# Kernel tuning notes

Measured on AMD Instinct MI355X. Metric: run time of the kernel, lower is better.

Reference implementation:

```python
import jax, jax.numpy as jnp
import numpy as np

LOG2E = 1.4426950408889634  # 1/ln(2): convert natural-log gates to log2 space (kernel uses exp2)
BT = 64  # chunk size


def setup_inputs() -> dict:
    key = jax.random.key(0)
    ks = jax.random.split(key, 5)
    B, H, T, K, V = 4, 8, 4096, 128, 128
    return {
        "q": jax.random.normal(ks[0], (B, H, T, K), dtype=jnp.float32),
        "k": jax.random.normal(ks[1], (B, H, T, K), dtype=jnp.float32),
        "v": jax.random.normal(ks[2], (B, H, T, V), dtype=jnp.float32),
        "i_gate": jax.random.normal(ks[3], (B, H, T), dtype=jnp.float32),
        "f_gate": jax.random.normal(ks[4], (B, H, T), dtype=jnp.float32),
    }


def reference(q, k, v, i_gate, f_gate):
    B, H, T, K = q.shape
    V = v.shape[-1]
    NT = T // BT
    scale = K ** -0.5

    # gate preprocessing: log-sigmoid forget gate, both gates moved to log2 space
    vecF = jax.nn.log_sigmoid(f_gate) * LOG2E  # [B,H,T]
    vecI = i_gate * LOG2E                      # [B,H,T]

    f_c = vecF.reshape(B, H, NT, BT)
    i_c = vecI.reshape(B, H, NT, BT)
    qc = q.reshape(B, H, NT, BT, K)
    kc = k.reshape(B, H, NT, BT, K)
    vc = v.reshape(B, H, NT, BT, V)

    vecB = jnp.cumsum(f_c, axis=-1)            # inclusive cumsum of f within chunk [B,H,NT,BT]
    scaG = vecB[..., -1]                       # total decay per chunk [B,H,NT]
    vecA = i_c + (scaG[..., None] - vecB)      # i_j + sum of f after j within chunk

    # ---- inter-chunk recurrence over matrix state C, normalizer n, max m ----
    kx = jnp.moveaxis(kc, 2, 0)  # [NT,B,H,BT,K]
    vx = jnp.moveaxis(vc, 2, 0)
    ax = jnp.moveaxis(vecA, 2, 0)  # [NT,B,H,BT]
    gx = jnp.moveaxis(scaG, 2, 0)  # [NT,B,H]

    C0 = jnp.zeros((B, H, K, V), dtype=q.dtype)
    n0 = jnp.zeros((B, H, K), dtype=q.dtype)
    m0 = jnp.zeros((B, H), dtype=q.dtype)

    def step(carry, inp):
        C, n, m = carry
        kk, vv, a, g = inp
        m_next = jnp.maximum(g + m, jnp.max(a, axis=-1))      # running stabilizer max
        dec = jnp.exp2(g + m - m_next)                        # [B,H]
        kbar = kk * jnp.exp2(a - m_next[..., None])[..., None]
        C_next = C * dec[..., None, None] + jnp.einsum('bhtk,bhtv->bhkv', kbar, vv)
        n_next = n * dec[..., None] + kbar.sum(axis=-2)
        return (C_next, n_next, m_next), (C, n, m)

    _, (Cp, np_, mp) = jax.lax.scan(step, (C0, n0, m0), (kx, vx, ax, gx))
    Cp = jnp.moveaxis(Cp, 0, 2)   # state entering each chunk [B,H,NT,K,V]
    np_ = jnp.moveaxis(np_, 0, 2)  # [B,H,NT,K]
    mp = jnp.moveaxis(mp, 0, 2)   # [B,H,NT]

    # ---- intra-chunk parallel part ----
    idx = jnp.arange(BT)
    causal = idx[:, None] >= idx[None, :]  # query i attends key j<=i
    # logD[i,j] = B_i - B_j + I_j for j<=i
    logD = vecB[..., :, None] - vecB[..., None, :] + i_c[..., None, :]
    logD = jnp.where(causal, logD, -jnp.inf)
    m_intra = logD.max(axis=-1)                                   # [B,H,NT,BT]
    m_comb = jnp.maximum(mp[..., None] + vecB, m_intra)           # total stabilizer per row
    D = jnp.exp2(logD - m_comb[..., None])                        # masked entries -> 0

    S = jnp.einsum('bhcik,bhcjk->bhcij', qc, kc) * scale * D
    qbar = qc * (scale * jnp.exp2(vecB + mp[..., None] - m_comb))[..., None]

    Hnum = jnp.einsum('bhcik,bhckv->bhciv', qbar, Cp) + jnp.einsum('bhcij,bhcjv->bhciv', S, vc)
    den = jnp.einsum('bhcik,bhck->bhci', qbar, np_) + S.sum(axis=-1)
    norm = jnp.maximum(jnp.abs(den), jnp.exp2(-m_comb))
    h = Hnum / norm[..., None]
    return h.reshape(B, H, T, V)
```

## Files before the change

kernel.cpp:

```cpp
#include <hip/hip_runtime.h>
#include <hip/hip_bf16.h>
#include <math.h>


#define LOG2E 1.4426950408889634f
constexpr int Bsz = 4, Hsz = 8, Tsz = 4096, Ksz = 128, Vsz = 128;
constexpr int BT = 64, NT = 64, BH = Bsz * Hsz;
constexpr float SCALE = 0.08838834764831845f;
constexpr int GS = 8, NG = NT / GS;

typedef __attribute__((ext_vector_type(8))) short short8v;
typedef __attribute__((ext_vector_type(4))) float f32x4;
typedef __attribute__((ext_vector_type(4))) unsigned short u16x4;
typedef __attribute__((ext_vector_type(8))) unsigned short u16x8;

__device__ inline float bf2f(unsigned short u) {
    union { unsigned int i; float f; } c; c.i = ((unsigned int)u) << 16; return c.f;
}
__device__ inline unsigned short f2bf(float f) {
    __hip_bfloat16 h = __float2bfloat16(f);
    union { __hip_bfloat16 b; unsigned short u; } cv; cv.b = h; return cv.u;
}
__device__ inline float f4c(const float4& v, int y) {
    return y == 0 ? v.x : y == 1 ? v.y : y == 2 ? v.z : v.w;
}

__global__ __launch_bounds__(64) void k_gates(
    const float* __restrict__ ig, const float* __restrict__ fg,
    float* __restrict__ vecB, float* __restrict__ vecI, float* __restrict__ vecA,
    float* __restrict__ mintra, float* __restrict__ scaG, float* __restrict__ scaA)
{
    int c = blockIdx.x, bh = blockIdx.y, lane = threadIdx.x;
    int t = bh * Tsz + c * BT + lane;
    float f = fg[t];
    float ls = fminf(f, 0.f) - log1pf(expf(-fabsf(f)));
    float vF = ls * LOG2E;
    float vI = ig[t] * LOG2E;
    float b = vF;
    #pragma unroll
    for (int off = 1; off < 64; off <<= 1) {
        float o = __shfl_up(b, off, 64);
        if (lane >= off) b += o;
    }
    float g = __shfl(b, 63, 64);
    float mi = vI - b;
    #pragma unroll
    for (int off = 1; off < 64; off <<= 1) {
        float o = __shfl_up(mi, off, 64);
        if (lane >= off) mi = fmaxf(mi, o);
    }
    float a = vI + g - b;
    vecB[t] = b; vecI[t] = vI; vecA[t] = a; mintra[t] = b + mi;
    float am = a;
    #pragma unroll
    for (int off = 32; off; off >>= 1) am = fmaxf(am, __shfl_xor(am, off, 64));
    if (lane == 0) { scaG[bh * NT + c] = g; scaA[bh * NT + c] = am; }
}

__global__ __launch_bounds__(64) void k_mscan(
    const float* __restrict__ scaG, const float* __restrict__ scaA,
    float* __restrict__ mp, float* __restrict__ dec,
    float* __restrict__ pdec, float* __restrict__ decG)
{
    int bh = blockIdx.x, lane = threadIdx.x;
    float g0 = scaG[bh * NT + lane];
    float a = g0, b = scaA[bh * NT + lane];
    #pragma unroll
    for (int off = 1; off < 64; off <<= 1) {
        float ap = __shfl_up(a, off, 64);
        float bp = __shfl_up(b, off, 64);
        if (lane >= off) { b = fmaxf(bp + a, b); a = ap + a; }
    }
    float m_incl = fmaxf(a, b);
    float m_prev = __shfl_up(m_incl, 1, 64);
    if (lane == 0) { m_prev = 0.f; mp[bh * (NT + 1)] = 0.f; }
    mp[bh * (NT + 1) + lane + 1] = m_incl;
    dec[bh * NT + lane] = exp2f(g0 + m_prev - m_incl);
    float cumE = a - g0;
    int gs = lane & ~(GS - 1);
    float cumE_gs = __shfl(cumE, gs, 64);
    float mp_gs   = __shfl(m_prev, gs, 64);
    pdec[bh * NT + lane] = exp2f(cumE - cumE_gs + mp_gs - m_prev);
    int ge = (lane * GS) & 63, gl = (lane * GS + GS - 1) & 63;
    float cumS = __shfl(cumE, ge, 64);
    float mS   = __shfl(m_prev, ge, 64);
    float cumL = __shfl(a, gl, 64);
    float mL   = __shfl(m_incl, gl, 64);
    if (lane < NG) decG[bh * NG + lane] = exp2f(cumL - cumS + mS - mL);
}

__global__ __launch_bounds__(256, 1) void k_state(
    const float* __restrict__ kg, const float* __restrict__ vg,
    const float* __restrict__ vecA, const float* __restrict__ mp,
    const float* __restrict__ dec,
    unsigned short* __restrict__ CpL, unsigned short* __restrict__ Gb,
    float* __restrict__ npl, float* __restrict__ nG)
{
    int g = blockIdx.x, bh = blockIdx.y, tid = threadIdx.x;
    int c0 = g * GS;
    int lane = tid & 63, wid = tid >> 6;
    int lrow = lane & 15, kgrp = lane >> 4;

    __shared__ __align__(16) unsigned short kT[2][128][72];
    __shared__ __align__(16) unsigned short vT[2][128][72];
    __shared__ float nUp[2][128][5];

    int cb = tid & 15, jr = tid >> 4;
    int wboff = (((jr >> 1) ^ (cb & 7)) * 16) + (jr & 1) * 8;
    const float* mpb = mp + bh * (NT + 1);

    float4 kreg[4][2], vreg[4][2];
    auto issue_loads = [&](int cc) {
        size_t hbc = (size_t)bh * Tsz + (size_t)(c0 + cc) * BT;
        #pragma unroll
        for (int x = 0; x < 4; ++x)
            #pragma unroll
            for (int p = 0; p < 2; ++p) {
                kreg[x][p] = *(const float4*)(kg + (hbc + jr * 4 + x) * Ksz + p * 64 + cb * 4);
                vreg[x][p] = *(const float4*)(vg + (hbc + jr * 4 + x) * Vsz + p * 64 + cb * 4);
            }
    };
    auto cvt_store = [&](int cc, int bb) {
        size_t hbc = (size_t)bh * Tsz + (size_t)(c0 + cc) * BT;
        float mpn = mpb[c0 + cc + 1];
        float s4[4];
        #pragma unroll
        for (int x = 0; x < 4; ++x) s4[x] = exp2f(vecA[hbc + jr * 4 + x] - mpn);
        #pragma unroll
        for (int p = 0; p < 2; ++p) {
            int cc0 = p * 64 + cb * 4;
            #pragma unroll
            for (int y = 0; y < 4; ++y) {
                u16x4 h, w;
                float psum = 0.f;
                #pragma unroll
                for (int x = 0; x < 4; ++x) {
                    float kf = f4c(kreg[x][p], y) * s4[x];
                    h[x] = f2bf(kf);
                    psum += kf;
                    w[x] = f2bf(f4c(vreg[x][p], y));
                }
                *(u16x4*)((char*)&kT[bb][cc0 + y][0] + wboff) = h;
                *(u16x4*)((char*)&vT[bb][cc0 + y][0] + wboff) = w;
                psum += __shfl_xor(psum, 16, 64);
                psum += __shfl_xor(psum, 32, 64);
                if (kgrp == 0) nUp[bb][cc0 + y][wid] = psum;
            }
        }
    };

    issue_loads(0);
    cvt_store(0, 0);
    __syncthreads();

    f32x4 acc[2][8];
    #pragma unroll
    for (int kt = 0; kt < 2; ++kt)
        #pragma unroll
        for (int vt = 0; vt < 8; ++vt) acc[kt][vt] = (f32x4){0.f, 0.f, 0.f, 0.f};
    float n_own = 0.f;

    int bb = 0;
    for (int t = 0; t < GS; ++t) {
        if (t + 1 < GS) issue_loads(t + 1);
        int c = c0 + t;
        unsigned short* Cb = CpL + (size_t)(bh * NT + c) * (Ksz * Vsz);
        #pragma unroll
        for (int kt = 0; kt < 2; ++kt) {
            int ktile = wid * 2 + kt;
            #pragma unroll
            for (int vt = 0; vt < 8; ++vt) {
                u16x4 w;
                #pragma unroll
                for (int r = 0; r < 4; ++r) w[r] = f2bf(acc[kt][vt][r]);
                *(u16x4*)(Cb + ((size_t)(ktile * 8 + vt) * 64 + lane) * 4) = w;
            }
        }
        if (tid < Ksz) npl[(size_t)(bh * NT + c) * Ksz + tid] = n_own;
        float dct = dec[bh * NT + c];
        #pragma unroll
        for (int kt = 0; kt < 2; ++kt)
            #pragma unroll
            for (int vt = 0; vt < 8; ++vt)
                #pragma unroll
                for (int r = 0; r < 4; ++r) acc[kt][vt][r] *= dct;
        #pragma unroll
        for (int ks = 0; ks < 2; ++ks) {
            int G2 = ks * 4 + kgrp;
            #pragma unroll
            for (int kt = 0; kt < 2; ++kt) {
                int arow = (wid * 2 + kt) * 16 + lrow;
                short8v af = *(const short8v*)((const char*)&kT[bb][arow][0]
                                               + ((G2 ^ ((arow >> 2) & 7)) * 16));
                #pragma unroll
                for (int vt = 0; vt < 8; ++vt) {
                    int brow = vt * 16 + lrow;
                    short8v bv = *(const short8v*)((const char*)&vT[bb][brow][0]
                                                   + ((G2 ^ ((brow >> 2) & 7)) * 16));
                    acc[kt][vt] = __builtin_amdgcn_mfma_f32_16x16x32_bf16(af, bv, acc[kt][vt], 0, 0, 0);
                }
            }
        }
        if (tid < Ksz) {
            float s = nUp[bb][tid][0] + nUp[bb][tid][1] + nUp[bb][tid][2] + nUp[bb][tid][3];
            n_own = n_own * dct + s;
        }
        if (t + 1 < GS) {
            cvt_store(t + 1, bb ^ 1);
            __syncthreads();
            bb ^= 1;
        }
    }
    unsigned short* Gg = Gb + (size_t)(bh * NG + g) * (Ksz * Vsz);
    #pragma unroll
    for (int kt = 0; kt < 2; ++kt) {
        int ktile = wid * 2 + kt;
        #pragma unroll
        for (int vt = 0; vt < 8; ++vt) {
            u16x4 w;
            #pragma unroll
            for (int r = 0; r < 4; ++r) w[r] = f2bf(acc[kt][vt][r]);
            *(u16x4*)(Gg + ((size_t)(ktile * 8 + vt) * 64 + lane) * 4) = w;
        }
    }
    if (tid < Ksz) nG[(size_t)(bh * NG + g) * Ksz + tid] = n_own;
}

__global__ __launch_bounds__(128) void k_gscan(
    unsigned short* __restrict__ Gb, float* __restrict__ nG,
    const float* __restrict__ decG)
{
    int s = blockIdx.x, bh = blockIdx.y, tid = threadIdx.x;
    __shared__ float dgs[NG];
    if (tid < NG) dgs[tid] = decG[bh * NG + tid];
    __syncthreads();
    if (s == 32) {
        float n = 0.f;
        size_t base = (size_t)bh * NG * Ksz + tid;
        #pragma unroll
        for (int g = 0; g < NG; ++g) {
            float u = nG[base + (size_t)g * Ksz];
            nG[base + (size_t)g * Ksz] = n;
            n = n * dgs[g] + u;
        }
        return;
    }
    size_t base = (size_t)bh * NG * (Ksz * Vsz) + s * 512 + tid * 4;
    float C0 = 0.f, C1 = 0.f, C2 = 0.f, C3 = 0.f;
    #pragma unroll
    for (int g = 0; g < NG; ++g) {
        size_t idx = base + (size_t)g * (Ksz * Vsz);
        u16x4 u = *(const u16x4*)(Gb + idx);
        u16x4 w;
        w.x = f2bf(C0); w.y = f2bf(C1); w.z = f2bf(C2); w.w = f2bf(C3);
        *(u16x4*)(Gb + idx) = w;
        float d = dgs[g];
        C0 = C0 * d + bf2f(u.x); C1 = C1 * d + bf2f(u.y);
        C2 = C2 * d + bf2f(u.z); C3 = C3 * d + bf2f(u.w);
    }
}

__global__ __launch_bounds__(256, 3) void k_intra(
    const float* __restrict__ qg, const float* __restrict__ kgl, const float* __restrict__ vg,
    const float* __restrict__ vecB, const float* __restrict__ vecI,
    const float* __restrict__ mintra, const float* __restrict__ mp,
    const float* __restrict__ npl, const float* __restrict__ nB,
    const unsigned short* __restrict__ CpL, const unsigned short* __restrict__ Bb,
    const float* __restrict__ pdec, float* __restrict__ out)
{
    int b0 = blockIdx.x, bh = blockIdx.y, tid = threadIdx.x;
    int c = ((b0 & 7) << 3) | (b0 >> 3);
    int lane = tid & 63, wid = tid >> 6;
    int lrow = lane & 15, kgrp = lane >> 4;
    int grp = c / GS;

    __shared__ __align__(16) unsigned short R[17408];
    __shared__ float rowf[BT], colf[BT], sfqs[BT], emcs[BT], denb[BT], npv[Ksz];

    auto khi = (unsigned short(*)[136])R;
    auto klo = (unsigned short(*)[136])(R + 64 * 136);
    auto Sb  = (unsigned short(*)[72])R;
    unsigned short* vTf = R + 64 * 72;
    unsigned short* cpsF = R;

    size_t hb = (size_t)bh * Tsz + (size_t)c * BT;
    float mpc = mp[bh * (NT + 1) + c];
    float pd = pdec[bh * NT + c];
    if (tid < BT) {
        float b = vecB[hb + tid];
        float mc = fmaxf(mpc + b, mintra[hb + tid]);
        rowf[tid] = SCALE * exp2f(b - mc);
        colf[tid] = exp2f(vecI[hb + tid] - b);
        sfqs[tid] = SCALE * exp2f(b + mpc - mc);
        emcs[tid] = exp2f(-mc);
    }
    if (tid < Ksz)
        npv[tid] = npl[((size_t)bh * NT + c) * Ksz + tid]
                 + pd * nB[((size_t)bh * NG + grp) * Ksz + tid];

    const float4* k4 = (const float4*)(kgl + hb * Ksz);
    for (int e = tid; e < BT * Ksz / 4; e += 256) {
        int i = e >> 5, c4 = (e & 31) * 4;
        float4 kv = k4[e];
        u16x4 h, l;
        h.x = f2bf(kv.x); l.x = f2bf(kv.x - bf2f(h.x));
        h.y = f2bf(kv.y); l.y = f2bf(kv.y - bf2f(h.y));
        h.z = f2bf(kv.z); l.z = f2bf(kv.z - bf2f(h.z));
        h.w = f2bf(kv.w); l.w = f2bf(kv.w - bf2f(h.w));
        *(u16x4*)&khi[i][c4] = h; *(u16x4*)&klo[i][c4] = l;
    }
    const float* qrow = qg + (hb + wid * 16 + lrow) * Ksz;
    float qf[4][8];
    #pragma unroll
    for (int ks = 0; ks < 4; ++ks) {
        float4 a = *(const float4*)(qrow + ks * 32 + kgrp * 8);
        float4 b = *(const float4*)(qrow + ks * 32 + kgrp * 8 + 4);
        qf[ks][0] = a.x; qf[ks][1] = a.y; qf[ks][2] = a.z; qf[ks][3] = a.w;
        qf[ks][4] = b.x; qf[ks][5] = b.y; qf[ks][6] = b.z; qf[ks][7] = b.w;
    }
    int vcb = tid & 15, jb = tid >> 4;
    float vpre[2][4][4];
    #pragma unroll
    for (int p = 0; p < 2; ++p)
        #pragma unroll
        for (int x = 0; x < 4; ++x) {
            float4 r4 = *(const float4*)(vg + (hb + jb * 4 + x) * Vsz + p * 64 + vcb * 4);
            vpre[p][x][0] = r4.x; vpre[p][x][1] = r4.y; vpre[p][x][2] = r4.z; vpre[p][x][3] = r4.w;
        }
    __syncthreads();

    float dot = 0.f;
    #pragma unroll
    for (int ks = 0; ks < 4; ++ks)
        #pragma unroll
        for (int x = 0; x < 8; ++x) dot += qf[ks][x] * npv[ks * 32 + kgrp * 8 + x];
    dot += __shfl_xor(dot, 16, 64);
    dot += __shfl_xor(dot, 32, 64);
    float qdot = sfqs[wid * 16 + lrow] * dot;

    short8v qh[4], ql[4];
    #pragma unroll
    for (int ks = 0; ks < 4; ++ks)
        #pragma unroll
        for (int x = 0; x < 8; ++x) {
            float f = qf[ks][x];
            unsigned short hh = f2bf(f);
            qh[ks][x] = (short)hh;
            ql[ks][x] = (short)f2bf(f - bf2f(hh));
        }

    f32x4 accS[4];
    #pragma unroll
    for (int jt = 0; jt < 4; ++jt) accS[jt] = (f32x4){0.f, 0.f, 0.f, 0.f};
    #pragma unroll
    for (int ks = 0; ks < 4; ++ks) {
        #pragma unroll
        for (int jt = 0; jt < 4; ++jt) {
            if (jt <= wid) {
                short8v bh_ = *(const short8v*)&khi[jt * 16 + lrow][ks * 32 + kgrp * 8];
                short8v bl  = *(const short8v*)&klo[jt * 16 + lrow][ks * 32 + kgrp * 8];
                accS[jt] = __builtin_amdgcn_mfma_f32_16x16x32_bf16(qh[ks], bh_, accS[jt], 0, 0, 0);
                accS[jt] = __builtin_amdgcn_mfma_f32_16x16x32_bf16(ql[ks], bh_, accS[jt], 0, 0, 0);
                accS[jt] = __builtin_amdgcn_mfma_f32_16x16x32_bf16(qh[ks], bl,  accS[jt], 0, 0, 0);
            }
        }
    }

    float rsum[4] = {0.f, 0.f, 0.f, 0.f};
    unsigned short sreg[4][4];
    #pragma unroll
    for (int jt = 0; jt < 4; ++jt)
        #pragma unroll
        for (int r = 0; r < 4; ++r) {
            int i = wid * 16 + kgrp * 4 + r, j = jt * 16 + lrow;
            float val = (j <= i) ? accS[jt][r] * rowf[i] * colf[j] : 0.f;
            rsum[r] += val;
            sreg[jt][r] = f2bf(val);
        }
    #pragma unroll
    for (int r = 0; r < 4; ++r) {
        rsum[r] += __shfl_xor(rsum[r], 1, 64);
        rsum[r] += __shfl_xor(rsum[r], 2, 64);
        rsum[r] += __shfl_xor(rsum[r], 4, 64);
        rsum[r] += __shfl_xor(rsum[r], 8, 64);
    }
    float qd[4];
    #pragma unroll
    for (int r = 0; r < 4; ++r) qd[r] = __shfl(qdot, kgrp * 4 + r, 64);
    if (lrow == 0) {
        #pragma unroll
        for (int r = 0; r < 4; ++r) {
            int i = wid * 16 + kgrp * 4 + r;
            float den = qd[r] + rsum[r];
            denb[i] = 1.f / fmaxf(fabsf(den), emcs[i]);
        }
    }
    __syncthreads();

    const u16x8* Cg = (const u16x8*)(CpL + ((size_t)bh * NT + c) * (Ksz * Vsz));
    const u16x8* Bg = (const u16x8*)(Bb + ((size_t)bh * NG + grp) * (Ksz * Vsz));
    u16x8 cpre[8], bpre[8];
    #pragma unroll
    for (int p2 = 0; p2 < 8; ++p2) { cpre[p2] = Cg[tid + p2 * 256]; bpre[p2] = Bg[tid + p2 * 256]; }

    #pragma unroll
    for (int jt = 0; jt < 4; ++jt)
        #pragma unroll
        for (int r = 0; r < 4; ++r)
            Sb[wid * 16 + kgrp * 4 + r][jt * 16 + lrow] = sreg[jt][r];
    #pragma unroll
    for (int p = 0; p < 2; ++p)
        #pragma unroll
        for (int y = 0; y < 4; ++y) {
            int row = p * 64 + vcb * 4 + y;
            int swzb = (jb * 8) ^ ((row & 7) << 4);
            u16x4 w;
            #pragma unroll
            for (int x = 0; x < 4; ++x) w[x] = f2bf(vpre[p][x][y]);
            *(u16x4*)((char*)(vTf + row * 64) + swzb) = w;
        }
    __syncthreads();

    f32x4 accV[8];
    #pragma unroll
    for (int vt = 0; vt < 8; ++vt) accV[vt] = (f32x4){0.f, 0.f, 0.f, 0.f};
    #pragma unroll
    for (int ks = 0; ks < 2; ++ks) {
        short8v as_ = *(const short8v*)&Sb[wid * 16 + lrow][ks * 32 + kgrp * 8];
        #pragma unroll
        for (int vt = 0; vt < 8; ++vt) {
            int row = vt * 16 + lrow;
            int swzb = ((ks * 64 + kgrp * 16)) ^ ((row & 7) << 4);
            short8v bv = *(const short8v*)((const char*)(vTf + row * 64) + swzb);
            accV[vt] = __builtin_amdgcn_mfma_f32_16x16x32_bf16(as_, bv, accV[vt], 0, 0, 0);
        }
    }
    __syncthreads();

    #pragma unroll
    for (int p2 = 0; p2 < 8; ++p2) {
        int idx = tid + p2 * 256;
        u16x8 cv = cpre[p2], bv = bpre[p2];
        u16x8 w;
        #pragma unroll
        for (int e = 0; e < 8; ++e) w[e] = f2bf(bf2f(cv[e]) + pd * bf2f(bv[e]));
        *(u16x8*)&cpsF[idx * 8] = w;
    }
    __syncthreads();

    f32x4 accC[8];
    #pragma unroll
    for (int vt = 0; vt < 8; ++vt) accC[vt] = (f32x4){0.f, 0.f, 0.f, 0.f};
    #pragma unroll
    for (int ks = 0; ks < 4; ++ks) {
        int ktile = ks * 2 + (kgrp >> 1);
        int lsrc = (kgrp & 1) * 32 + lrow;
        #pragma unroll
        for (int vt = 0; vt < 8; ++vt) {
            const unsigned short* pf = &cpsF[((ktile * 8 + vt) * 64 + lsrc) * 4];
            u16x4 lo4 = *(const u16x4*)pf;
            u16x4 hi4 = *(const u16x4*)(pf + 64);
            short8v bc;
            bc[0] = (short)lo4.x; bc[1] = (short)lo4.y; bc[2] = (short)lo4.z; bc[3] = (short)lo4.w;
            bc[4] = (short)hi4.x; bc[5] = (short)hi4.y; bc[6] = (short)hi4.z; bc[7] = (short)hi4.w;
            accC[vt] = __builtin_amdgcn_mfma_f32_16x16x32_bf16(qh[ks], bc, accC[vt], 0, 0, 0);
            accC[vt] = __builtin_amdgcn_mfma_f32_16x16x32_bf16(ql[ks], bc, accC[vt], 0, 0, 0);
        }
    }
    size_t gb = hb * Vsz;
    #pragma unroll
    for (int vt = 0; vt < 8; ++vt)
        #pragma unroll
        for (int r = 0; r < 4; ++r) {
            int i = wid * 16 + kgrp * 4 + r, vc = vt * 16 + lrow;
            out[gb + (size_t)i * Vsz + vc] = (sfqs[i] * accC[vt][r] + accV[vt][r]) * denb[i];
        }
}

extern "C" void kernel_launch(void* const* d_in, const int* in_sizes, int n_in,
                              void* d_out, int out_size, void* d_ws, size_t ws_size,
                              hipStream_t stream) {
    const float* q  = (const float*)d_in[0];
    const float* k  = (const float*)d_in[1];
    const float* v  = (const float*)d_in[2];
    const float* ig = (const float*)d_in[3];
    const float* fg = (const float*)d_in[4];
    float* out = (float*)d_out;

    float* ws = (float*)d_ws;
    float* vecB   = ws;
    float* vecI   = vecB + BH * Tsz;
    float* vecA   = vecI + BH * Tsz;
    float* mintra = vecA + BH * Tsz;
    float* scaG   = mintra + BH * Tsz;
    float* scaA   = scaG + BH * NT;
    float* dec    = scaA + BH * NT;
    float* pdec   = dec + BH * NT;
    float* decG   = pdec + BH * NT;
    float* mp     = decG + BH * NG;
    float* npl    = mp + BH * (NT + 1);
    float* nG     = npl + BH * NT * Ksz;
    unsigned short* CpL = (unsigned short*)(nG + BH * NG * Ksz);
    unsigned short* Gb  = CpL + (size_t)BH * NT * Ksz * Vsz;

    k_gates<<<dim3(NT, BH), 64, 0, stream>>>(ig, fg, vecB, vecI, vecA, mintra, scaG, scaA);
    k_mscan<<<dim3(BH), 64, 0, stream>>>(scaG, scaA, mp, dec, pdec, decG);
    k_state<<<dim3(NG, BH), 256, 0, stream>>>(k, v, vecA, mp, dec, CpL, Gb, npl, nG);
    k_gscan<<<dim3(33, BH), 128, 0, stream>>>(Gb, nG, decG);
    k_intra<<<dim3(NT, BH), 256, 0, stream>>>(q, k, v, vecB, vecI, mintra, mp,
                                              npl, nG, CpL, Gb, pdec, out);
}
```

Measured before the change: 119.2 us.

## Split k_state across V halves to double grid parallelism

The state-accumulation kernel now launches a third grid dimension that splits the V dimension into two halves. Each block loads only its half of v and keeps half the accumulators, which doubles the block count from 256 to 512 on a GPU with many CUs. The cost is that k is loaded, scaled and converted twice, and the normalizer is computed redundantly, with only one half writing it. Launch bounds for k_state become 2 and for k_intra drop from 3 to 2, which changes register budgets.

```diff
diff --git a/kernel.cpp b/kernel.cpp
--- a/kernel.cpp
+++ b/kernel.cpp
@@ -89,36 +89,36 @@
     if (lane < NG) decG[bh * NG + lane] = exp2f(cumL - cumS + mS - mL);
 }
 
-__global__ __launch_bounds__(256, 1) void k_state(
+__global__ __launch_bounds__(256, 2) void k_state(
     const float* __restrict__ kg, const float* __restrict__ vg,
     const float* __restrict__ vecA, const float* __restrict__ mp,
     const float* __restrict__ dec,
     unsigned short* __restrict__ CpL, unsigned short* __restrict__ Gb,
     float* __restrict__ npl, float* __restrict__ nG)
 {
-    int g = blockIdx.x, bh = blockIdx.y, tid = threadIdx.x;
+    int g = blockIdx.x, bh = blockIdx.y, vhalf = blockIdx.z, tid = threadIdx.x;
     int c0 = g * GS;
     int lane = tid & 63, wid = tid >> 6;
     int lrow = lane & 15, kgrp = lane >> 4;
 
     __shared__ __align__(16) unsigned short kT[2][128][72];
-    __shared__ __align__(16) unsigned short vT[2][128][72];
+    __shared__ __align__(16) unsigned short vT[2][64][72];
     __shared__ float nUp[2][128][5];
 
     int cb = tid & 15, jr = tid >> 4;
     int wboff = (((jr >> 1) ^ (cb & 7)) * 16) + (jr & 1) * 8;
     const float* mpb = mp + bh * (NT + 1);
 
-    float4 kreg[4][2], vreg[4][2];
+    float4 kreg[4][2], vreg[4];
     auto issue_loads = [&](int cc) {
         size_t hbc = (size_t)bh * Tsz + (size_t)(c0 + cc) * BT;
         #pragma unroll
-        for (int x = 0; x < 4; ++x)
-            #pragma unroll
-            for (int p = 0; p < 2; ++p) {
+        for (int x = 0; x < 4; ++x) {
+            #pragma unroll
+            for (int p = 0; p < 2; ++p)
                 kreg[x][p] = *(const float4*)(kg + (hbc + jr * 4 + x) * Ksz + p * 64 + cb * 4);
-                vreg[x][p] = *(const float4*)(vg + (hbc + jr * 4 + x) * Vsz + p * 64 + cb * 4);
-            }
+            vreg[x] = *(const float4*)(vg + (hbc + jr * 4 + x) * Vsz + vhalf * 64 + cb * 4);
+        }
     };
     auto cvt_store = [&](int cc, int bb) {
         size_t hbc = (size_t)bh * Tsz + (size_t)(c0 + cc) * BT;
@@ -131,33 +131,38 @@
             int cc0 = p * 64 + cb * 4;
             #pragma unroll
             for (int y = 0; y < 4; ++y) {
-                u16x4 h, w;
+                u16x4 h;
                 float psum = 0.f;
                 #pragma unroll
                 for (int x = 0; x < 4; ++x) {
                     float kf = f4c(kreg[x][p], y) * s4[x];
                     h[x] = f2bf(kf);
                     psum += kf;
-                    w[x] = f2bf(f4c(vreg[x][p], y));
                 }
                 *(u16x4*)((char*)&kT[bb][cc0 + y][0] + wboff) = h;
-                *(u16x4*)((char*)&vT[bb][cc0 + y][0] + wboff) = w;
                 psum += __shfl_xor(psum, 16, 64);
                 psum += __shfl_xor(psum, 32, 64);
                 if (kgrp == 0) nUp[bb][cc0 + y][wid] = psum;
             }
         }
+        #pragma unroll
+        for (int y = 0; y < 4; ++y) {
+            u16x4 w;
+            #pragma unroll
+            for (int x = 0; x < 4; ++x) w[x] = f2bf(f4c(vreg[x], y));
+            *(u16x4*)((char*)&vT[bb][cb * 4 + y][0] + wboff) = w;
+        }
     };
 
     issue_loads(0);
     cvt_store(0, 0);
     __syncthreads();
 
-    f32x4 acc[2][8];
+    f32x4 acc[2][4];
     #pragma unroll
     for (int kt = 0; kt < 2; ++kt)
         #pragma unroll
-        for (int vt = 0; vt < 8; ++vt) acc[kt][vt] = (f32x4){0.f, 0.f, 0.f, 0.f};
+        for (int vt = 0; vt < 4; ++vt) acc[kt][vt] = (f32x4){0.f, 0.f, 0.f, 0.f};
     float n_own = 0.f;
 
     int bb = 0;
@@ -169,19 +174,19 @@
         for (int kt = 0; kt < 2; ++kt) {
             int ktile = wid * 2 + kt;
             #pragma unroll
-            for (int vt = 0; vt < 8; ++vt) {
+            for (int vt = 0; vt < 4; ++vt) {
                 u16x4 w;
                 #pragma unroll
                 for (int r = 0; r < 4; ++r) w[r] = f2bf(acc[kt][vt][r]);
-                *(u16x4*)(Cb + ((size_t)(ktile * 8 + vt) * 64 + lane) * 4) = w;
+                *(u16x4*)(Cb + ((size_t)(ktile * 8 + vhalf * 4 + vt) * 64 + lane) * 4) = w;
             }
         }
-        if (tid < Ksz) npl[(size_t)(bh * NT + c) * Ksz + tid] = n_own;
+        if (vhalf == 0 && tid < Ksz) npl[(size_t)(bh * NT + c) * Ksz + tid] = n_own;
         float dct = dec[bh * NT + c];
         #pragma unroll
         for (int kt = 0; kt < 2; ++kt)
             #pragma unroll
-            for (int vt = 0; vt < 8; ++vt)
+            for (int vt = 0; vt < 4; ++vt)
                 #pragma unroll
                 for (int r = 0; r < 4; ++r) acc[kt][vt][r] *= dct;
         #pragma unroll
@@ -193,7 +198,7 @@
                 short8v af = *(const short8v*)((const char*)&kT[bb][arow][0]
                                                + ((G2 ^ ((arow >> 2) & 7)) * 16));
                 #pragma unroll
-                for (int vt = 0; vt < 8; ++vt) {
+                for (int vt = 0; vt < 4; ++vt) {
                     int brow = vt * 16 + lrow;
                     short8v bv = *(const short8v*)((const char*)&vT[bb][brow][0]
                                                    + ((G2 ^ ((brow >> 2) & 7)) * 16));
@@ -216,14 +221,14 @@
     for (int kt = 0; kt < 2; ++kt) {
         int ktile = wid * 2 + kt;
         #pragma unroll
-        for (int vt = 0; vt < 8; ++vt) {
+        for (int vt = 0; vt < 4; ++vt) {
             u16x4 w;
             #pragma unroll
             for (int r = 0; r < 4; ++r) w[r] = f2bf(acc[kt][vt][r]);
-            *(u16x4*)(Gg + ((size_t)(ktile * 8 + vt) * 64 + lane) * 4) = w;
-        }
-    }
-    if (tid < Ksz) nG[(size_t)(bh * NG + g) * Ksz + tid] = n_own;
+            *(u16x4*)(Gg + ((size_t)(ktile * 8 + vhalf * 4 + vt) * 64 + lane) * 4) = w;
+        }
+    }
+    if (vhalf == 0 && tid < Ksz) nG[(size_t)(bh * NG + g) * Ksz + tid] = n_own;
 }
 
 __global__ __launch_bounds__(128) void k_gscan(
@@ -260,7 +265,7 @@
     }
 }
 
-__global__ __launch_bounds__(256, 3) void k_intra(
+__global__ __launch_bounds__(256, 2) void k_intra(
     const float* __restrict__ qg, const float* __restrict__ kgl, const float* __restrict__ vg,
     const float* __restrict__ vecB, const float* __restrict__ vecI,
     const float* __restrict__ mintra, const float* __restrict__ mp,
@@ -505,7 +510,7 @@
 
     k_gates<<<dim3(NT, BH), 64, 0, stream>>>(ig, fg, vecB, vecI, vecA, mintra, scaG, scaA);
     k_mscan<<<dim3(BH), 64, 0, stream>>>(scaG, scaA, mp, dec, pdec, decG);
-    k_state<<<dim3(NG, BH), 256, 0, stream>>>(k, v, vecA, mp, dec, CpL, Gb, npl, nG);
+    k_state<<<dim3(NG, BH, 2), 256, 0, stream>>>(k, v, vecA, mp, dec, CpL, Gb, npl, nG);
     k_gscan<<<dim3(33, BH), 128, 0, stream>>>(Gb, nG, decG);
     k_intra<<<dim3(NT, BH), 256, 0, stream>>>(q, k, v, vecB, vecI, mintra, mp,
                                               npl, nG, CpL, Gb, pdec, out);
```

Result: faster. 116.5 us (-2.3%).
